# Kernel tuning notes

Measured on AMD Instinct MI355X. Metric: run time of the kernel, lower is better.

## Reference

```python
import jax, jax.numpy as jnp
import numpy as np

B, T, C, HD = 4, 2048, 1024, 64

def setup_inputs() -> dict:
    key = jax.random.key(0)
    kx, kq, kk, kv = jax.random.split(key, 4)
    # Weights stored as [n_embed, head_size]; equivalent to torch Linear weight transposed.
    scale = 1.0 / np.sqrt(C)
    return {
        "x": jax.random.normal(kx, (B, T, C), dtype=jnp.float32),
        "Wq": jax.random.normal(kq, (C, HD), dtype=jnp.float32) * scale,
        "Wk": jax.random.normal(kk, (C, HD), dtype=jnp.float32) * scale,
        "Wv": jax.random.normal(kv, (C, HD), dtype=jnp.float32) * scale,
    }

def reference(x, Wq, Wk, Wv):
    # Projections (no bias)
    q = x @ Wq  # [B,T,HD]
    k = x @ Wk
    v = x @ Wv
    hd = k.shape[-1]
    # NOTE: original multiplies by sqrt(head_size) (not the usual 1/sqrt) -- faithful.
    scores = jnp.einsum("btd,bsd->bts", q, k) * (hd ** 0.5)  # [B,T,T]
    # First softmax over full (unmasked) rows
    w = jax.nn.softmax(scores, axis=-1)
    # Causal mask applied AFTER the first softmax, then a second softmax
    causal = jnp.tril(jnp.ones((q.shape[1], q.shape[1]), dtype=bool))  # [T,T]
    w = jnp.where(causal[None, :, :], w, -jnp.inf)
    w = jax.nn.softmax(w, axis=-1)
    out = jnp.einsum("bts,bsd->btd", w, v)  # [B,T,HD]
    return out
```

## Files before the change

kernel.cpp:

```cpp
#include <hip/hip_runtime.h>
#include <math.h>

#define T_  2048
#define C_  1024
#define HD_ 64
#define BB_ 4

typedef __attribute__((ext_vector_type(8))) short bf16x8;
typedef __attribute__((ext_vector_type(4))) float f32x4;

#define MFMA_BF16(A, B, C) __builtin_amdgcn_mfma_f32_16x16x32_bf16(A, B, C, 0, 0, 0)

__device__ __forceinline__ short f2bf(float f) {
    union { float f; unsigned u; } v; v.f = f;
    unsigned r = v.u + 0x7fffu + ((v.u >> 16) & 1u);
    return (short)(r >> 16);
}
__device__ __forceinline__ float bf2f(short s) {
    union { float f; unsigned u; } v;
    v.u = ((unsigned)(unsigned short)s) << 16;
    return v.f;
}

__global__ __launch_bounds__(256) void prep_w_kernel(
    const float* __restrict__ Wq, const float* __restrict__ Wk,
    const float* __restrict__ Wv, short* __restrict__ wt)
{
    const int m = blockIdx.y;
    const float* W = (m == 0) ? Wq : (m == 1) ? Wk : Wv;
    const int t = threadIdx.x;
    const int c = blockIdx.x * 64 + (t >> 2);
    const int hg = (t & 3) * 16;
    const float4* wp = (const float4*)(W + (size_t)c * HD_ + hg);
    short* hi = wt + (size_t)(m * 2 + 0) * 64 * 1024;
    short* lo = wt + (size_t)(m * 2 + 1) * 64 * 1024;
    #pragma unroll
    for (int u = 0; u < 4; ++u) {
        float4 f = wp[u];
        float vv0 = f.x, vv1 = f.y, vv2 = f.z, vv3 = f.w;
        float vs[4] = {vv0, vv1, vv2, vv3};
        #pragma unroll
        for (int e = 0; e < 4; ++e) {
            int h = hg + u * 4 + e;
            short hh = f2bf(vs[e]);
            short ll = f2bf(vs[e] - bf2f(hh));
            hi[(size_t)h * 1024 + c] = hh;
            lo[(size_t)h * 1024 + c] = ll;
        }
    }
}

__global__ __launch_bounds__(256) void qkv_proj_kernel(
    const float* __restrict__ x, const short* __restrict__ wt,
    short* __restrict__ qhp, short* __restrict__ qlp,
    short* __restrict__ khp, short* __restrict__ klp,
    short* __restrict__ vtp)
{
    __shared__ __align__(16) short xh[64 * 64], xl[64 * 64];
    __shared__ __align__(16) short wh[64 * 64], wl[64 * 64];

    const int t  = threadIdx.x;
    const int L  = t & 63;
    const int wv = t >> 6;
    const int m  = blockIdx.y;
    const int R0 = blockIdx.x * 64;

    const int xt0 = (wv & 1) * 2;
    const int wt0 = (wv >> 1) * 2;

    f32x4 acc[2][2];
    #pragma unroll
    for (int i = 0; i < 2; ++i)
        #pragma unroll
        for (int j = 0; j < 2; ++j)
            acc[i][j] = {0.f, 0.f, 0.f, 0.f};

    const int sr  = t & 63;
    const int scg = t >> 6;

    for (int c0 = 0; c0 < C_; c0 += 64) {
        __syncthreads();
        {
            const float4* xp = (const float4*)(x + (size_t)(R0 + sr) * C_ + c0 + scg * 16);
            #pragma unroll
            for (int g = 0; g < 2; ++g) {
                bf16x8 vh, vl;
                #pragma unroll
                for (int u = 0; u < 2; ++u) {
                    float4 f = xp[g * 2 + u];
                    float vs[4] = {f.x, f.y, f.z, f.w};
                    #pragma unroll
                    for (int e = 0; e < 4; ++e) {
                        short hh = f2bf(vs[e]);
                        vh[u * 4 + e] = hh;
                        vl[u * 4 + e] = f2bf(vs[e] - bf2f(hh));
                    }
                }
                int ch = scg * 2 + g;
                int off = sr * 64 + ((ch ^ (sr & 7)) * 8);
                *(bf16x8*)&xh[off] = vh;
                *(bf16x8*)&xl[off] = vl;
            }
        }
        {
            const int pl = t >> 7;
            const int id = t & 127;
            const short* wsrc = wt + (size_t)(m * 2 + pl) * 64 * 1024;
            short* wdst = pl ? wl : wh;
            #pragma unroll
            for (int u = 0; u < 4; ++u) {
                int cid = id * 4 + u;
                int h = cid >> 3, c8 = cid & 7;
                bf16x8 v = *(const bf16x8*)(wsrc + (size_t)h * 1024 + c0 + c8 * 8);
                *(bf16x8*)&wdst[h * 64 + ((c8 ^ (h & 7)) * 8)] = v;
            }
        }
        __syncthreads();
        #pragma unroll
        for (int kc = 0; kc < 2; ++kc) {
            bf16x8 ax[2], axl[2], bw[2], bwl[2];
            #pragma unroll
            for (int i = 0; i < 2; ++i) {
                int row = (xt0 + i) * 16 + (L & 15);
                int ch  = kc * 4 + (L >> 4);
                int off = row * 64 + ((ch ^ (row & 7)) * 8);
                ax[i]  = *(const bf16x8*)&xh[off];
                axl[i] = *(const bf16x8*)&xl[off];
                int hrow = (wt0 + i) * 16 + (L & 15);
                int off2 = hrow * 64 + ((ch ^ (hrow & 7)) * 8);
                bw[i]  = *(const bf16x8*)&wh[off2];
                bwl[i] = *(const bf16x8*)&wl[off2];
            }
            if (m < 2) {
                #pragma unroll
                for (int i = 0; i < 2; ++i)
                    #pragma unroll
                    for (int j = 0; j < 2; ++j) {
                        acc[i][j] = MFMA_BF16(axl[i], bw[j], acc[i][j]);
                        acc[i][j] = MFMA_BF16(ax[i], bwl[j], acc[i][j]);
                        acc[i][j] = MFMA_BF16(ax[i], bw[j], acc[i][j]);
                    }
            } else {
                #pragma unroll
                for (int i = 0; i < 2; ++i)
                    #pragma unroll
                    for (int j = 0; j < 2; ++j) {
                        acc[i][j] = MFMA_BF16(bwl[j], ax[i], acc[i][j]);
                        acc[i][j] = MFMA_BF16(bw[j], axl[i], acc[i][j]);
                        acc[i][j] = MFMA_BF16(bw[j], ax[i], acc[i][j]);
                    }
            }
        }
    }

    if (m < 2) {
        short* ph = (m == 0) ? qhp : khp;
        short* pl = (m == 0) ? qlp : klp;
        const float sc = (m == 0) ? 8.f : 1.f;
        #pragma unroll
        for (int i = 0; i < 2; ++i)
            #pragma unroll
            for (int j = 0; j < 2; ++j)
                #pragma unroll
                for (int r = 0; r < 4; ++r) {
                    int row = R0 + (xt0 + i) * 16 + (L >> 4) * 4 + r;
                    int h   = (wt0 + j) * 16 + (L & 15);
                    float v = acc[i][j][r] * sc;
                    short hh = f2bf(v);
                    ph[(size_t)row * HD_ + h] = hh;
                    pl[(size_t)row * HD_ + h] = f2bf(v - bf2f(hh));
                }
    } else {
        #pragma unroll
        for (int i = 0; i < 2; ++i)
            #pragma unroll
            for (int j = 0; j < 2; ++j)
                #pragma unroll
                for (int r = 0; r < 4; ++r) {
                    int d  = (wt0 + j) * 16 + (L >> 4) * 4 + r;
                    int tt = R0 + (xt0 + i) * 16 + (L & 15);
                    int bb = tt >> 11, tl = tt & (T_ - 1);
                    vtp[(size_t)(bb * 64 + d) * T_ + tl] = f2bf(acc[i][j][r]);
                }
    }
}

__global__ __launch_bounds__(512) void attn_kernel(
    const short* __restrict__ qhp, const short* __restrict__ qlp,
    const short* __restrict__ khp, const short* __restrict__ klp,
    const short* __restrict__ vtp, float* __restrict__ out)
{
    __shared__ __align__(16) short khs[128 * 64];
    __shared__ __align__(16) short kls[128 * 64];
    __shared__ __align__(16) short vts[64 * 128];
    __shared__ __align__(16) short ebs[32 * 128];
    __shared__ float red[8 * 32 * 2];
    __shared__ float mrow[32], ilrow[32], dinv[32];

    const int t  = threadIdx.x;
    const int L  = t & 63;
    const int wv = t >> 6;
    const int b  = blockIdx.x >> 6;
    const int p  = blockIdx.x & 63;
    const int IA = p * 16, IB = (127 - p) * 16;

    bf16x8 qfh[2][2], qfl[2][2];
    #pragma unroll
    for (int rt = 0; rt < 2; ++rt) {
        int row = (rt ? IB : IA) + (L & 15);
        const short* qb  = qhp + ((size_t)b * T_ + row) * HD_;
        const short* qbl = qlp + ((size_t)b * T_ + row) * HD_;
        #pragma unroll
        for (int dc = 0; dc < 2; ++dc) {
            int off = dc * 32 + (L >> 4) * 8;
            qfh[rt][dc] = *(const bf16x8*)(qb + off);
            qfl[rt][dc] = *(const bf16x8*)(qbl + off);
        }
    }

    const short* kbh = khp + (size_t)b * T_ * HD_;
    const short* kbl = klp + (size_t)b * T_ * HD_;
    const short* vb  = vtp + (size_t)b * 64 * T_;

    const int spl = t >> 8;
    const int sid = t & 255;

    auto stageK = [&](int jt) {
        const short* src = spl ? kbl : kbh;
        short* dst = spl ? kls : khs;
        #pragma unroll
        for (int u = 0; u < 4; ++u) {
            int cid = sid * 4 + u;
            int col = cid >> 3, c8 = cid & 7;
            bf16x8 v = *(const bf16x8*)(src + (size_t)(jt * 128 + col) * HD_ + c8 * 8);
            *(bf16x8*)&dst[col * 64 + ((c8 ^ (col & 7)) * 8)] = v;
        }
    };
    auto stageV = [&](int jt) {
        #pragma unroll
        for (int u = 0; u < 2; ++u) {
            int cid = t + u * 512;
            int d = cid >> 4, ch = cid & 15;
            bf16x8 v = *(const bf16x8*)(vb + (size_t)d * T_ + jt * 128 + ch * 8);
            *(bf16x8*)&vts[d * 128 + ((ch ^ ((d & 7) * 2)) * 8)] = v;
        }
    };

    float ml[2][4], ll[2][4];
    #pragma unroll
    for (int rt = 0; rt < 2; ++rt)
        #pragma unroll
        for (int r = 0; r < 4; ++r) { ml[rt][r] = -1e30f; ll[rt][r] = 0.f; }

    for (int jt = 0; jt < 16; ++jt) {
        __syncthreads();
        stageK(jt);
        __syncthreads();
        const int col = wv * 16 + (L & 15);
        bf16x8 kf[2], kfl[2];
        #pragma unroll
        for (int dc = 0; dc < 2; ++dc) {
            int ch = dc * 4 + (L >> 4);
            int off = col * 64 + ((ch ^ (col & 7)) * 8);
            kf[dc]  = *(const bf16x8*)&khs[off];
            kfl[dc] = *(const bf16x8*)&kls[off];
        }
        #pragma unroll
        for (int rt = 0; rt < 2; ++rt) {
            f32x4 s = {0.f, 0.f, 0.f, 0.f};
            #pragma unroll
            for (int dc = 0; dc < 2; ++dc) {
                s = MFMA_BF16(qfl[rt][dc], kf[dc], s);
                s = MFMA_BF16(qfh[rt][dc], kfl[dc], s);
                s = MFMA_BF16(qfh[rt][dc], kf[dc], s);
            }
            #pragma unroll
            for (int r = 0; r < 4; ++r) {
                float sv = s[r];
                float mn = fmaxf(ml[rt][r], sv);
                ll[rt][r] = ll[rt][r] * __expf(ml[rt][r] - mn) + __expf(sv - mn);
                ml[rt][r] = mn;
            }
        }
    }
    #pragma unroll
    for (int off = 1; off < 16; off <<= 1)
        #pragma unroll
        for (int rt = 0; rt < 2; ++rt)
            #pragma unroll
            for (int r = 0; r < 4; ++r) {
                float mo = __shfl_xor(ml[rt][r], off, 64);
                float lo = __shfl_xor(ll[rt][r], off, 64);
                float mn = fmaxf(ml[rt][r], mo);
                ll[rt][r] = ll[rt][r] * __expf(ml[rt][r] - mn) + lo * __expf(mo - mn);
                ml[rt][r] = mn;
            }
    if ((L & 15) == 0) {
        #pragma unroll
        for (int rt = 0; rt < 2; ++rt)
            #pragma unroll
            for (int r = 0; r < 4; ++r) {
                int rid = rt * 16 + (L >> 4) * 4 + r;
                red[(wv * 32 + rid) * 2 + 0] = ml[rt][r];
                red[(wv * 32 + rid) * 2 + 1] = ll[rt][r];
            }
    }
    __syncthreads();
    if (t < 32) {
        float M = red[t * 2], S = red[t * 2 + 1];
        #pragma unroll
        for (int w = 1; w < 8; ++w) {
            float mo = red[(w * 32 + t) * 2], lo = red[(w * 32 + t) * 2 + 1];
            float mn = fmaxf(M, mo);
            S = S * __expf(M - mn) + lo * __expf(mo - mn);
            M = mn;
        }
        mrow[t] = M;
        ilrow[t] = 1.f / S;
    }
    __syncthreads();

    float ms[2][4], is[2][4];
    int rowg[2][4];
    #pragma unroll
    for (int rt = 0; rt < 2; ++rt)
        #pragma unroll
        for (int r = 0; r < 4; ++r) {
            int rid = rt * 16 + (L >> 4) * 4 + r;
            ms[rt][r] = mrow[rid];
            is[rt][r] = ilrow[rid];
            rowg[rt][r] = (rt ? IB : IA) + (L >> 4) * 4 + r;
        }

    const int nA = (IA + 143) >> 7;
    const int nB = (IB + 143) >> 7;
    const int rtp = wv & 1, dh = (wv >> 1) & 1, khf = wv >> 2;
    f32x4 ov[2];
    ov[0] = {0.f, 0.f, 0.f, 0.f};
    ov[1] = {0.f, 0.f, 0.f, 0.f};
    float dn[2][4];
    #pragma unroll
    for (int rt = 0; rt < 2; ++rt)
        #pragma unroll
        for (int r = 0; r < 4; ++r) dn[rt][r] = 0.f;

    for (int jt = 0; jt < nB; ++jt) {
        __syncthreads();
        stageK(jt);
        stageV(jt);
        __syncthreads();
        const int col = wv * 16 + (L & 15);
        bf16x8 kf[2], kfl[2];
        #pragma unroll
        for (int dc = 0; dc < 2; ++dc) {
            int ch = dc * 4 + (L >> 4);
            int off = col * 64 + ((ch ^ (col & 7)) * 8);
            kf[dc]  = *(const bf16x8*)&khs[off];
            kfl[dc] = *(const bf16x8*)&kls[off];
        }
        for (int rt = 0; rt < 2; ++rt) {
            if (rt == 0 && jt >= nA) continue;
            f32x4 s = {0.f, 0.f, 0.f, 0.f};
            #pragma unroll
            for (int dc = 0; dc < 2; ++dc) {
                s = MFMA_BF16(qfl[rt][dc], kf[dc], s);
                s = MFMA_BF16(qfh[rt][dc], kfl[dc], s);
                s = MFMA_BF16(qfh[rt][dc], kf[dc], s);
            }
            #pragma unroll
            for (int r = 0; r < 4; ++r) {
                float pv = __expf(s[r] - ms[rt][r]) * is[rt][r];
                int colg = jt * 128 + col;
                float ev = (colg <= rowg[rt][r]) ? __expf(pv) : 0.f;
                short e16 = f2bf(ev);
                dn[rt][r] += bf2f(e16);
                int rid = rt * 16 + (L >> 4) * 4 + r;
                ebs[rid * 128 + (((col >> 3) ^ ((rid & 7) * 2)) * 8) + (col & 7)] = e16;
            }
        }
        __syncthreads();
        if (!(rtp == 0 && jt >= nA)) {
            #pragma unroll
            for (int u = 0; u < 2; ++u) {
                int kc = khf * 2 + u;
                int rid = rtp * 16 + (L & 15);
                int ch = kc * 4 + (L >> 4);
                bf16x8 ef = *(const bf16x8*)&ebs[rid * 128 + ((ch ^ ((rid & 7) * 2)) * 8)];
                #pragma unroll
                for (int dt = 0; dt < 2; ++dt) {
                    int d = dh * 32 + dt * 16 + (L & 15);
                    bf16x8 vf = *(const bf16x8*)&vts[d * 128 + ((ch ^ ((d & 7) * 2)) * 8)];
                    ov[dt] = MFMA_BF16(ef, vf, ov[dt]);
                }
            }
        }
    }

    #pragma unroll
    for (int off = 1; off < 16; off <<= 1)
        #pragma unroll
        for (int rt = 0; rt < 2; ++rt)
            #pragma unroll
            for (int r = 0; r < 4; ++r)
                dn[rt][r] += __shfl_xor(dn[rt][r], off, 64);
    __syncthreads();
    if ((L & 15) == 0) {
        #pragma unroll
        for (int rt = 0; rt < 2; ++rt)
            #pragma unroll
            for (int r = 0; r < 4; ++r) {
                int rid = rt * 16 + (L >> 4) * 4 + r;
                red[wv * 32 + rid] = dn[rt][r];
            }
    }
    __syncthreads();
    if (t < 32) {
        float D = 0.f;
        #pragma unroll
        for (int w = 0; w < 8; ++w) D += red[w * 32 + t];
        dinv[t] = 1.f / D;
    }
    float* obuf = (float*)ebs;
    __syncthreads();
    if (khf == 1) {
        #pragma unroll
        for (int dt = 0; dt < 2; ++dt)
            #pragma unroll
            for (int r = 0; r < 4; ++r)
                obuf[((wv - 4) * 64 + L) * 8 + dt * 4 + r] = ov[dt][r];
    }
    __syncthreads();
    if (khf == 0) {
        float* ob = out + (size_t)b * T_ * HD_;
        #pragma unroll
        for (int dt = 0; dt < 2; ++dt)
            #pragma unroll
            for (int r = 0; r < 4; ++r) {
                float o = ov[dt][r] + obuf[(wv * 64 + L) * 8 + dt * 4 + r];
                int rid = rtp * 16 + (L >> 4) * 4 + r;
                int row = (rtp ? IB : IA) + (L >> 4) * 4 + r;
                int d = dh * 32 + dt * 16 + (L & 15);
                ob[(size_t)row * HD_ + d] = o * dinv[rid];
            }
    }
}

extern "C" void kernel_launch(void* const* d_in, const int* in_sizes, int n_in,
                              void* d_out, int out_size, void* d_ws, size_t ws_size,
                              hipStream_t stream) {
    (void)in_sizes; (void)n_in; (void)out_size; (void)ws_size;
    const float* x  = (const float*)d_in[0];
    const float* Wq = (const float*)d_in[1];
    const float* Wk = (const float*)d_in[2];
    const float* Wv = (const float*)d_in[3];
    float* outp = (float*)d_out;

    char* ws = (char*)d_ws;
    short* wt = (short*)ws;
    short* qh = (short*)(ws + 786432);
    short* ql = (short*)(ws + 786432 + 1048576);
    short* kh = (short*)(ws + 786432 + 2 * 1048576);
    short* kl = (short*)(ws + 786432 + 3 * 1048576);
    short* vt = (short*)(ws + 786432 + 4 * 1048576);

    prep_w_kernel<<<dim3(16, 3), 256, 0, stream>>>(Wq, Wk, Wv, wt);
    qkv_proj_kernel<<<dim3(128, 3), 256, 0, stream>>>(x, wt, qh, ql, kh, kl, vt);
    attn_kernel<<<dim3(256), 512, 0, stream>>>(qh, ql, kh, kl, vt, outp);
}
```

Measured before the change: 157.3 us.

## Split attention into parallel stats, merge and PV kernels; fuse QKV projection

The QKV projection now computes Q, K and V together in one block over 32-row tiles, so each x tile is loaded and converted to bf16 hi/lo once, with register prefetch of the next tile. V uses a single bf16 MFMA instead of three. The full-row softmax statistics move out of the attention kernel into a separate stats kernel that splits key segments across more blocks, followed by a small merge kernel, and the PV kernel reads the precomputed max and inverse sum. The exp buffer is now kept in fp32 shared memory and converted at MFMA load time. This trades two extra launches, an extra K pass and a larger shared footprint for more parallelism in the statistics pass, and V loses its bf16 low-part precision.

```diff
diff --git a/kernel.cpp b/kernel.cpp
--- a/kernel.cpp
+++ b/kernel.cpp
@@ -4,7 +4,6 @@
 #define T_  2048
 #define C_  1024
 #define HD_ 64
-#define BB_ 4
 
 typedef __attribute__((ext_vector_type(8))) short bf16x8;
 typedef __attribute__((ext_vector_type(4))) float f32x4;
@@ -37,15 +36,13 @@
     #pragma unroll
     for (int u = 0; u < 4; ++u) {
         float4 f = wp[u];
-        float vv0 = f.x, vv1 = f.y, vv2 = f.z, vv3 = f.w;
-        float vs[4] = {vv0, vv1, vv2, vv3};
+        float vs[4] = {f.x, f.y, f.z, f.w};
         #pragma unroll
         for (int e = 0; e < 4; ++e) {
             int h = hg + u * 4 + e;
             short hh = f2bf(vs[e]);
-            short ll = f2bf(vs[e] - bf2f(hh));
             hi[(size_t)h * 1024 + c] = hh;
-            lo[(size_t)h * 1024 + c] = ll;
+            lo[(size_t)h * 1024 + c] = f2bf(vs[e] - bf2f(hh));
         }
     }
 }
@@ -56,217 +53,180 @@
     short* __restrict__ khp, short* __restrict__ klp,
     short* __restrict__ vtp)
 {
-    __shared__ __align__(16) short xh[64 * 64], xl[64 * 64];
-    __shared__ __align__(16) short wh[64 * 64], wl[64 * 64];
-
-    const int t  = threadIdx.x;
-    const int L  = t & 63;
-    const int wv = t >> 6;
-    const int m  = blockIdx.y;
-    const int R0 = blockIdx.x * 64;
-
-    const int xt0 = (wv & 1) * 2;
-    const int wt0 = (wv >> 1) * 2;
-
-    f32x4 acc[2][2];
+    __shared__ __align__(16) short xh[32 * 64], xl[32 * 64];
+    __shared__ __align__(16) short wh[192 * 64], wl[192 * 64];
+
+    const int t = threadIdx.x, L = t & 63, wv = t >> 6;
+    const int R0 = blockIdx.x * 32;
+    const int xrow = t >> 3, xch = t & 7;
+
+    f32x4 acc[2][3];
     #pragma unroll
     for (int i = 0; i < 2; ++i)
         #pragma unroll
-        for (int j = 0; j < 2; ++j)
-            acc[i][j] = {0.f, 0.f, 0.f, 0.f};
-
-    const int sr  = t & 63;
-    const int scg = t >> 6;
-
+        for (int j = 0; j < 3; ++j) acc[i][j] = {0.f, 0.f, 0.f, 0.f};
+
+    float4 xa0, xa1;
+    bf16x8 wr[2][6];
+    const float* xp = x + (size_t)(R0 + xrow) * C_ + xch * 8;
+
+    auto loadX = [&](int c0) {
+        xa0 = *(const float4*)(xp + c0);
+        xa1 = *(const float4*)(xp + c0 + 4);
+    };
+    auto loadW = [&](int c0) {
+        #pragma unroll
+        for (int pl = 0; pl < 2; ++pl)
+            #pragma unroll
+            for (int u = 0; u < 6; ++u) {
+                int cc = t + 256 * u;
+                int row = cc >> 3, ch = cc & 7;
+                int m = row >> 6, h = row & 63;
+                wr[pl][u] = *(const bf16x8*)(wt + (size_t)(m * 2 + pl) * 65536
+                                             + (size_t)h * 1024 + c0 + ch * 8);
+            }
+    };
+
+    loadX(0); loadW(0);
     for (int c0 = 0; c0 < C_; c0 += 64) {
         __syncthreads();
         {
-            const float4* xp = (const float4*)(x + (size_t)(R0 + sr) * C_ + c0 + scg * 16);
-            #pragma unroll
-            for (int g = 0; g < 2; ++g) {
-                bf16x8 vh, vl;
+            float vs[8] = {xa0.x, xa0.y, xa0.z, xa0.w, xa1.x, xa1.y, xa1.z, xa1.w};
+            bf16x8 vh, vl;
+            #pragma unroll
+            for (int e = 0; e < 8; ++e) {
+                short hh = f2bf(vs[e]);
+                vh[e] = hh;
+                vl[e] = f2bf(vs[e] - bf2f(hh));
+            }
+            int slot = (xch ^ (xrow & 7)) * 8;
+            *(bf16x8*)&xh[xrow * 64 + slot] = vh;
+            *(bf16x8*)&xl[xrow * 64 + slot] = vl;
+        }
+        {
+            #pragma unroll
+            for (int pl = 0; pl < 2; ++pl)
                 #pragma unroll
-                for (int u = 0; u < 2; ++u) {
-                    float4 f = xp[g * 2 + u];
-                    float vs[4] = {f.x, f.y, f.z, f.w};
-                    #pragma unroll
-                    for (int e = 0; e < 4; ++e) {
-                        short hh = f2bf(vs[e]);
-                        vh[u * 4 + e] = hh;
-                        vl[u * 4 + e] = f2bf(vs[e] - bf2f(hh));
-                    }
+                for (int u = 0; u < 6; ++u) {
+                    int cc = t + 256 * u;
+                    int row = cc >> 3, ch = cc & 7;
+                    short* dst = pl ? wl : wh;
+                    *(bf16x8*)&dst[row * 64 + ((ch ^ (row & 7)) * 8)] = wr[pl][u];
                 }
-                int ch = scg * 2 + g;
-                int off = sr * 64 + ((ch ^ (sr & 7)) * 8);
-                *(bf16x8*)&xh[off] = vh;
-                *(bf16x8*)&xl[off] = vl;
-            }
-        }
+        }
+        if (c0 + 64 < C_) { loadX(c0 + 64); loadW(c0 + 64); }
+        __syncthreads();
+        #pragma unroll
+        for (int kc = 0; kc < 2; ++kc) {
+            const int ch = kc * 4 + (L >> 4);
+            bf16x8 axh[2], axl[2], bwh[3], bwl[3];
+            #pragma unroll
+            for (int rt = 0; rt < 2; ++rt) {
+                int row = rt * 16 + (L & 15);
+                int off = row * 64 + ((ch ^ (row & 7)) * 8);
+                axh[rt] = *(const bf16x8*)&xh[off];
+                axl[rt] = *(const bf16x8*)&xl[off];
+            }
+            #pragma unroll
+            for (int cl = 0; cl < 3; ++cl) {
+                int ct = wv + cl * 4;
+                int wrow = ct * 16 + (L & 15);
+                int off = wrow * 64 + ((ch ^ (wrow & 7)) * 8);
+                bwh[cl] = *(const bf16x8*)&wh[off];
+                bwl[cl] = *(const bf16x8*)&wl[off];
+            }
+            #pragma unroll
+            for (int rt = 0; rt < 2; ++rt) {
+                acc[rt][0] = MFMA_BF16(axl[rt], bwh[0], acc[rt][0]);
+                acc[rt][0] = MFMA_BF16(axh[rt], bwl[0], acc[rt][0]);
+                acc[rt][0] = MFMA_BF16(axh[rt], bwh[0], acc[rt][0]);
+                acc[rt][1] = MFMA_BF16(axl[rt], bwh[1], acc[rt][1]);
+                acc[rt][1] = MFMA_BF16(axh[rt], bwl[1], acc[rt][1]);
+                acc[rt][1] = MFMA_BF16(axh[rt], bwh[1], acc[rt][1]);
+                acc[rt][2] = MFMA_BF16(bwh[2], axh[rt], acc[rt][2]);
+            }
+        }
+    }
+
+    const int quad = L >> 4;
+    #pragma unroll
+    for (int rt = 0; rt < 2; ++rt) {
+        #pragma unroll
+        for (int r = 0; r < 4; ++r) {
+            int row = R0 + rt * 16 + quad * 4 + r;
+            int h = wv * 16 + (L & 15);
+            float vq = acc[rt][0][r] * 8.f;
+            short hq = f2bf(vq);
+            qhp[(size_t)row * HD_ + h] = hq;
+            qlp[(size_t)row * HD_ + h] = f2bf(vq - bf2f(hq));
+            float vk = acc[rt][1][r];
+            short hk = f2bf(vk);
+            khp[(size_t)row * HD_ + h] = hk;
+            klp[(size_t)row * HD_ + h] = f2bf(vk - bf2f(hk));
+            int d = wv * 16 + quad * 4 + r;
+            int tt = R0 + rt * 16 + (L & 15);
+            int bb = tt >> 11, tl = tt & (T_ - 1);
+            vtp[(size_t)(bb * 64 + d) * T_ + tl] = f2bf(acc[rt][2][r]);
+        }
+    }
+}
+
+__global__ __launch_bounds__(256) void stats_kernel(
+    const short* __restrict__ qhp, const short* __restrict__ qlp,
+    const short* __restrict__ khp, const short* __restrict__ klp,
+    float* __restrict__ pm)
+{
+    __shared__ __align__(16) short khs[64 * 64], kls[64 * 64];
+    __shared__ float red[4 * 64 * 2];
+
+    const int t = threadIdx.x, L = t & 63, wv = t >> 6;
+    const int bt = blockIdx.x, seg = blockIdx.y, b = blockIdx.z;
+    const int R0 = bt * 64, S0 = seg * 512;
+
+    bf16x8 qfh[4][2], qfl[4][2];
+    #pragma unroll
+    for (int rt = 0; rt < 4; ++rt)
+        #pragma unroll
+        for (int dc = 0; dc < 2; ++dc) {
+            int row = R0 + rt * 16 + (L & 15);
+            size_t off = ((size_t)b * T_ + row) * HD_ + dc * 32 + (L >> 4) * 8;
+            qfh[rt][dc] = *(const bf16x8*)(qhp + off);
+            qfl[rt][dc] = *(const bf16x8*)(qlp + off);
+        }
+
+    float ml[4][4], ll[4][4];
+    #pragma unroll
+    for (int rt = 0; rt < 4; ++rt)
+        #pragma unroll
+        for (int r = 0; r < 4; ++r) { ml[rt][r] = -1e30f; ll[rt][r] = 0.f; }
+
+    const int pl = t >> 7, id = t & 127;
+    for (int jt = 0; jt < 8; ++jt) {
+        __syncthreads();
         {
-            const int pl = t >> 7;
-            const int id = t & 127;
-            const short* wsrc = wt + (size_t)(m * 2 + pl) * 64 * 1024;
-            short* wdst = pl ? wl : wh;
+            const short* src = pl ? klp : khp;
+            short* dst = pl ? kls : khs;
             #pragma unroll
             for (int u = 0; u < 4; ++u) {
                 int cid = id * 4 + u;
-                int h = cid >> 3, c8 = cid & 7;
-                bf16x8 v = *(const bf16x8*)(wsrc + (size_t)h * 1024 + c0 + c8 * 8);
-                *(bf16x8*)&wdst[h * 64 + ((c8 ^ (h & 7)) * 8)] = v;
-            }
-        }
-        __syncthreads();
-        #pragma unroll
-        for (int kc = 0; kc < 2; ++kc) {
-            bf16x8 ax[2], axl[2], bw[2], bwl[2];
-            #pragma unroll
-            for (int i = 0; i < 2; ++i) {
-                int row = (xt0 + i) * 16 + (L & 15);
-                int ch  = kc * 4 + (L >> 4);
-                int off = row * 64 + ((ch ^ (row & 7)) * 8);
-                ax[i]  = *(const bf16x8*)&xh[off];
-                axl[i] = *(const bf16x8*)&xl[off];
-                int hrow = (wt0 + i) * 16 + (L & 15);
-                int off2 = hrow * 64 + ((ch ^ (hrow & 7)) * 8);
-                bw[i]  = *(const bf16x8*)&wh[off2];
-                bwl[i] = *(const bf16x8*)&wl[off2];
-            }
-            if (m < 2) {
-                #pragma unroll
-                for (int i = 0; i < 2; ++i)
-                    #pragma unroll
-                    for (int j = 0; j < 2; ++j) {
-                        acc[i][j] = MFMA_BF16(axl[i], bw[j], acc[i][j]);
-                        acc[i][j] = MFMA_BF16(ax[i], bwl[j], acc[i][j]);
-                        acc[i][j] = MFMA_BF16(ax[i], bw[j], acc[i][j]);
-                    }
-            } else {
-                #pragma unroll
-                for (int i = 0; i < 2; ++i)
-                    #pragma unroll
-                    for (int j = 0; j < 2; ++j) {
-                        acc[i][j] = MFMA_BF16(bwl[j], ax[i], acc[i][j]);
-                        acc[i][j] = MFMA_BF16(bw[j], axl[i], acc[i][j]);
-                        acc[i][j] = MFMA_BF16(bw[j], ax[i], acc[i][j]);
-                    }
-            }
-        }
-    }
-
-    if (m < 2) {
-        short* ph = (m == 0) ? qhp : khp;
-        short* pl = (m == 0) ? qlp : klp;
-        const float sc = (m == 0) ? 8.f : 1.f;
-        #pragma unroll
-        for (int i = 0; i < 2; ++i)
-            #pragma unroll
-            for (int j = 0; j < 2; ++j)
-                #pragma unroll
-                for (int r = 0; r < 4; ++r) {
-                    int row = R0 + (xt0 + i) * 16 + (L >> 4) * 4 + r;
-                    int h   = (wt0 + j) * 16 + (L & 15);
-                    float v = acc[i][j][r] * sc;
-                    short hh = f2bf(v);
-                    ph[(size_t)row * HD_ + h] = hh;
-                    pl[(size_t)row * HD_ + h] = f2bf(v - bf2f(hh));
-                }
-    } else {
-        #pragma unroll
-        for (int i = 0; i < 2; ++i)
-            #pragma unroll
-            for (int j = 0; j < 2; ++j)
-                #pragma unroll
-                for (int r = 0; r < 4; ++r) {
-                    int d  = (wt0 + j) * 16 + (L >> 4) * 4 + r;
-                    int tt = R0 + (xt0 + i) * 16 + (L & 15);
-                    int bb = tt >> 11, tl = tt & (T_ - 1);
-                    vtp[(size_t)(bb * 64 + d) * T_ + tl] = f2bf(acc[i][j][r]);
-                }
-    }
-}
-
-__global__ __launch_bounds__(512) void attn_kernel(
-    const short* __restrict__ qhp, const short* __restrict__ qlp,
-    const short* __restrict__ khp, const short* __restrict__ klp,
-    const short* __restrict__ vtp, float* __restrict__ out)
-{
-    __shared__ __align__(16) short khs[128 * 64];
-    __shared__ __align__(16) short kls[128 * 64];
-    __shared__ __align__(16) short vts[64 * 128];
-    __shared__ __align__(16) short ebs[32 * 128];
-    __shared__ float red[8 * 32 * 2];
-    __shared__ float mrow[32], ilrow[32], dinv[32];
-
-    const int t  = threadIdx.x;
-    const int L  = t & 63;
-    const int wv = t >> 6;
-    const int b  = blockIdx.x >> 6;
-    const int p  = blockIdx.x & 63;
-    const int IA = p * 16, IB = (127 - p) * 16;
-
-    bf16x8 qfh[2][2], qfl[2][2];
-    #pragma unroll
-    for (int rt = 0; rt < 2; ++rt) {
-        int row = (rt ? IB : IA) + (L & 15);
-        const short* qb  = qhp + ((size_t)b * T_ + row) * HD_;
-        const short* qbl = qlp + ((size_t)b * T_ + row) * HD_;
-        #pragma unroll
-        for (int dc = 0; dc < 2; ++dc) {
-            int off = dc * 32 + (L >> 4) * 8;
-            qfh[rt][dc] = *(const bf16x8*)(qb + off);
-            qfl[rt][dc] = *(const bf16x8*)(qbl + off);
-        }
-    }
-
-    const short* kbh = khp + (size_t)b * T_ * HD_;
-    const short* kbl = klp + (size_t)b * T_ * HD_;
-    const short* vb  = vtp + (size_t)b * 64 * T_;
-
-    const int spl = t >> 8;
-    const int sid = t & 255;
-
-    auto stageK = [&](int jt) {
-        const short* src = spl ? kbl : kbh;
-        short* dst = spl ? kls : khs;
-        #pragma unroll
-        for (int u = 0; u < 4; ++u) {
-            int cid = sid * 4 + u;
-            int col = cid >> 3, c8 = cid & 7;
-            bf16x8 v = *(const bf16x8*)(src + (size_t)(jt * 128 + col) * HD_ + c8 * 8);
-            *(bf16x8*)&dst[col * 64 + ((c8 ^ (col & 7)) * 8)] = v;
-        }
-    };
-    auto stageV = [&](int jt) {
-        #pragma unroll
-        for (int u = 0; u < 2; ++u) {
-            int cid = t + u * 512;
-            int d = cid >> 4, ch = cid & 15;
-            bf16x8 v = *(const bf16x8*)(vb + (size_t)d * T_ + jt * 128 + ch * 8);
-            *(bf16x8*)&vts[d * 128 + ((ch ^ ((d & 7) * 2)) * 8)] = v;
-        }
-    };
-
-    float ml[2][4], ll[2][4];
-    #pragma unroll
-    for (int rt = 0; rt < 2; ++rt)
-        #pragma unroll
-        for (int r = 0; r < 4; ++r) { ml[rt][r] = -1e30f; ll[rt][r] = 0.f; }
-
-    for (int jt = 0; jt < 16; ++jt) {
-        __syncthreads();
-        stageK(jt);
-        __syncthreads();
-        const int col = wv * 16 + (L & 15);
+                int col = cid >> 3, ch = cid & 7;
+                bf16x8 v = *(const bf16x8*)(src
+                    + ((size_t)b * T_ + S0 + jt * 64 + col) * HD_ + ch * 8);
+                *(bf16x8*)&dst[col * 64 + ((ch ^ (col & 7)) * 8)] = v;
+            }
+        }
+        __syncthreads();
+        const int colL = wv * 16 + (L & 15);
         bf16x8 kf[2], kfl[2];
         #pragma unroll
         for (int dc = 0; dc < 2; ++dc) {
             int ch = dc * 4 + (L >> 4);
-            int off = col * 64 + ((ch ^ (col & 7)) * 8);
+            int off = colL * 64 + ((ch ^ (colL & 7)) * 8);
             kf[dc]  = *(const bf16x8*)&khs[off];
             kfl[dc] = *(const bf16x8*)&kls[off];
         }
         #pragma unroll
-        for (int rt = 0; rt < 2; ++rt) {
+        for (int rt = 0; rt < 4; ++rt) {
             f32x4 s = {0.f, 0.f, 0.f, 0.f};
             #pragma unroll
             for (int dc = 0; dc < 2; ++dc) {
@@ -276,9 +236,8 @@
             }
             #pragma unroll
             for (int r = 0; r < 4; ++r) {
-                float sv = s[r];
-                float mn = fmaxf(ml[rt][r], sv);
-                ll[rt][r] = ll[rt][r] * __expf(ml[rt][r] - mn) + __expf(sv - mn);
+                float mn = fmaxf(ml[rt][r], s[r]);
+                ll[rt][r] = ll[rt][r] * __expf(ml[rt][r] - mn) + __expf(s[r] - mn);
                 ml[rt][r] = mn;
             }
         }
@@ -286,7 +245,7 @@
     #pragma unroll
     for (int off = 1; off < 16; off <<= 1)
         #pragma unroll
-        for (int rt = 0; rt < 2; ++rt)
+        for (int rt = 0; rt < 4; ++rt)
             #pragma unroll
             for (int r = 0; r < 4; ++r) {
                 float mo = __shfl_xor(ml[rt][r], off, 64);
@@ -297,40 +256,113 @@
             }
     if ((L & 15) == 0) {
         #pragma unroll
-        for (int rt = 0; rt < 2; ++rt)
+        for (int rt = 0; rt < 4; ++rt)
             #pragma unroll
             for (int r = 0; r < 4; ++r) {
-                int rid = rt * 16 + (L >> 4) * 4 + r;
-                red[(wv * 32 + rid) * 2 + 0] = ml[rt][r];
-                red[(wv * 32 + rid) * 2 + 1] = ll[rt][r];
+                int row = rt * 16 + (L >> 4) * 4 + r;
+                red[(wv * 64 + row) * 2 + 0] = ml[rt][r];
+                red[(wv * 64 + row) * 2 + 1] = ll[rt][r];
             }
     }
     __syncthreads();
-    if (t < 32) {
+    if (t < 64) {
         float M = red[t * 2], S = red[t * 2 + 1];
         #pragma unroll
-        for (int w = 1; w < 8; ++w) {
-            float mo = red[(w * 32 + t) * 2], lo = red[(w * 32 + t) * 2 + 1];
+        for (int w = 1; w < 4; ++w) {
+            float mo = red[(w * 64 + t) * 2], lo = red[(w * 64 + t) * 2 + 1];
             float mn = fmaxf(M, mo);
             S = S * __expf(M - mn) + lo * __expf(mo - mn);
             M = mn;
         }
-        mrow[t] = M;
-        ilrow[t] = 1.f / S;
-    }
-    __syncthreads();
-
+        size_t o = ((size_t)((b * 32 + bt) * 4 + seg) * 64 + t) * 2;
+        pm[o] = M;
+        pm[o + 1] = S;
+    }
+}
+
+__global__ __launch_bounds__(256) void stat_merge_kernel(
+    const float* __restrict__ pm, float* __restrict__ msp, float* __restrict__ ilp)
+{
+    int gid = blockIdx.x * 256 + threadIdx.x;
+    int b = gid >> 11, rl = gid & 2047, bt = rl >> 6, rr = rl & 63;
+    float M = -1e30f, S = 0.f;
+    #pragma unroll
+    for (int seg = 0; seg < 4; ++seg) {
+        size_t o = ((size_t)((b * 32 + bt) * 4 + seg) * 64 + rr) * 2;
+        float mo = pm[o], lo = pm[o + 1];
+        float mn = fmaxf(M, mo);
+        S = S * __expf(M - mn) + lo * __expf(mo - mn);
+        M = mn;
+    }
+    msp[gid] = M;
+    ilp[gid] = 1.f / S;
+}
+
+__global__ __launch_bounds__(512) void pv_kernel(
+    const short* __restrict__ qhp, const short* __restrict__ qlp,
+    const short* __restrict__ khp, const short* __restrict__ klp,
+    const short* __restrict__ vtp, const float* __restrict__ msp,
+    const float* __restrict__ ilp, float* __restrict__ out)
+{
+    __shared__ __align__(16) short khs[128 * 64];
+    __shared__ __align__(16) short kls[128 * 64];
+    __shared__ __align__(16) short vts[64 * 128];
+    __shared__ __align__(16) float es[32 * 128];
+
+    const int t = threadIdx.x, L = t & 63, wv = t >> 6;
+    const int b = blockIdx.x >> 6, p = blockIdx.x & 63;
+    const int IA = p * 16, IB = (127 - p) * 16;
+
+    bf16x8 qfh[2][2], qfl[2][2];
+    #pragma unroll
+    for (int rt = 0; rt < 2; ++rt) {
+        int row = (rt ? IB : IA) + (L & 15);
+        const short* qb  = qhp + ((size_t)b * T_ + row) * HD_;
+        const short* qbl = qlp + ((size_t)b * T_ + row) * HD_;
+        #pragma unroll
+        for (int dc = 0; dc < 2; ++dc) {
+            int off = dc * 32 + (L >> 4) * 8;
+            qfh[rt][dc] = *(const bf16x8*)(qb + off);
+            qfl[rt][dc] = *(const bf16x8*)(qbl + off);
+        }
+    }
     float ms[2][4], is[2][4];
     int rowg[2][4];
     #pragma unroll
     for (int rt = 0; rt < 2; ++rt)
         #pragma unroll
         for (int r = 0; r < 4; ++r) {
-            int rid = rt * 16 + (L >> 4) * 4 + r;
-            ms[rt][r] = mrow[rid];
-            is[rt][r] = ilrow[rid];
-            rowg[rt][r] = (rt ? IB : IA) + (L >> 4) * 4 + r;
-        }
+            int rg = (rt ? IB : IA) + (L >> 4) * 4 + r;
+            rowg[rt][r] = rg;
+            ms[rt][r] = msp[b * T_ + rg];
+            is[rt][r] = ilp[b * T_ + rg];
+        }
+
+    const short* kbh = khp + (size_t)b * T_ * HD_;
+    const short* kbl = klp + (size_t)b * T_ * HD_;
+    const short* vb  = vtp + (size_t)b * 64 * T_;
+    const int spl = t >> 8, sid = t & 255;
+
+    auto stageK = [&](int jt) {
+        const short* src = spl ? kbl : kbh;
+        short* dst = spl ? kls : khs;
+        #pragma unroll
+        for (int u = 0; u < 4; ++u) {
+            int cid = sid * 4 + u;
+            int col = cid >> 3, c8 = cid & 7;
+            bf16x8 v = *(const bf16x8*)(src + (size_t)(jt * 128 + col) * HD_ + c8 * 8);
+            *(bf16x8*)&dst[col * 64 + ((c8 ^ (col & 7)) * 8)] = v;
+        }
+    };
+    auto stageV = [&](int jt) {
+        #pragma unroll
+        for (int u = 0; u < 2; ++u) {
+            int cid = t + u * 512;
+            int d = cid >> 4, ch = cid & 15;
+            bf16x8 v = *(const bf16x8*)(vb + (size_t)d * T_ + jt * 128 + ch * 8);
+            *(bf16x8*)&vts[d * 128 + ((ch ^ ((d & 7) * 2)) * 8)] = v;
+        }
+    };
 
     const int nA = (IA + 143) >> 7;
     const int nB = (IB + 143) >> 7;
@@ -372,10 +404,9 @@
                 float pv = __expf(s[r] - ms[rt][r]) * is[rt][r];
                 int colg = jt * 128 + col;
                 float ev = (colg <= rowg[rt][r]) ? __expf(pv) : 0.f;
-                short e16 = f2bf(ev);
-                dn[rt][r] += bf2f(e16);
+                dn[rt][r] += ev;
                 int rid = rt * 16 + (L >> 4) * 4 + r;
-                ebs[rid * 128 + (((col >> 3) ^ ((rid & 7) * 2)) * 8) + (col & 7)] = e16;
+                es[rid * 128 + (((col >> 3) ^ (rid & 15)) * 8) + (col & 7)] = ev;
             }
         }
         __syncthreads();
@@ -384,11 +415,19 @@
             for (int u = 0; u < 2; ++u) {
                 int kc = khf * 2 + u;
                 int rid = rtp * 16 + (L & 15);
-                int ch = kc * 4 + (L >> 4);
-                bf16x8 ef = *(const bf16x8*)&ebs[rid * 128 + ((ch ^ ((rid & 7) * 2)) * 8)];
+                int chunk = (kc * 4 + (L >> 4)) ^ (rid & 15);
+                const float* ep = &es[rid * 128 + chunk * 8];
+                float4 e0 = *(const float4*)ep;
+                float4 e1 = *(const float4*)(ep + 4);
+                bf16x8 ef;
+                ef[0] = f2bf(e0.x); ef[1] = f2bf(e0.y);
+                ef[2] = f2bf(e0.z); ef[3] = f2bf(e0.w);
+                ef[4] = f2bf(e1.x); ef[5] = f2bf(e1.y);
+                ef[6] = f2bf(e1.z); ef[7] = f2bf(e1.w);
                 #pragma unroll
                 for (int dt = 0; dt < 2; ++dt) {
                     int d = dh * 32 + dt * 16 + (L & 15);
+                    int ch = kc * 4 + (L >> 4);
                     bf16x8 vf = *(const bf16x8*)&vts[d * 128 + ((ch ^ ((d & 7) * 2)) * 8)];
                     ov[dt] = MFMA_BF16(ef, vf, ov[dt]);
                 }
@@ -404,6 +443,8 @@
             for (int r = 0; r < 4; ++r)
                 dn[rt][r] += __shfl_xor(dn[rt][r], off, 64);
     __syncthreads();
+    float* red  = es + 2304;
+    float* dinv = es + 2560;
     if ((L & 15) == 0) {
         #pragma unroll
         for (int rt = 0; rt < 2; ++rt)
@@ -420,7 +461,7 @@
         for (int w = 0; w < 8; ++w) D += red[w * 32 + t];
         dinv[t] = 1.f / D;
     }
-    float* obuf = (float*)ebs;
+    float* obuf = es;
     __syncthreads();
     if (khf == 1) {
         #pragma unroll
@@ -456,7 +497,10 @@
     float* outp = (float*)d_out;
 
     char* ws = (char*)d_ws;
-    short* wt = (short*)ws;
+    short* wt  = (short*)ws;
+    float* pm  = (float*)ws;
+    float* msp = (float*)(ws + 262144);
+    float* ilp = (float*)(ws + 294912);
     short* qh = (short*)(ws + 786432);
     short* ql = (short*)(ws + 786432 + 1048576);
     short* kh = (short*)(ws + 786432 + 2 * 1048576);
@@ -464,6 +508,8 @@
     short* vt = (short*)(ws + 786432 + 4 * 1048576);
 
     prep_w_kernel<<<dim3(16, 3), 256, 0, stream>>>(Wq, Wk, Wv, wt);
-    qkv_proj_kernel<<<dim3(128, 3), 256, 0, stream>>>(x, wt, qh, ql, kh, kl, vt);
-    attn_kernel<<<dim3(256), 512, 0, stream>>>(qh, ql, kh, kl, vt, outp);
-}
+    qkv_proj_kernel<<<dim3(256), 256, 0, stream>>>(x, wt, qh, ql, kh, kl, vt);
+    stats_kernel<<<dim3(32, 4, 4), 256, 0, stream>>>(qh, ql, kh, kl, pm);
+    stat_merge_kernel<<<dim3(32), 256, 0, stream>>>(pm, msp, ilp);
+    pv_kernel<<<dim3(256), 512, 0, stream>>>(qh, ql, kh, kl, vt, msp, ilp, outp);
+}
```

Measured after the change: 155.8 us. Within noise of the previous version (-1.0%).
